# Optimization experiments

Hardware: AMD Instinct MI355X
Metric: run time of the kernel (lower is better)

The kernel has to match this reference:

```python
import jax, jax.numpy as jnp
import numpy as np

EPS = 1e-6
PRED_LEN = 336
K_DETACH = 6

def expmap0(v):
    # tangent v [..., E] at Lorentz origin (k=1) -> point [..., E+1]
    r = jnp.linalg.norm(v, axis=-1, keepdims=True)
    x0 = jnp.cosh(r)
    scale = jnp.where(r > EPS, jnp.sinh(r) / jnp.maximum(r, EPS), 1.0)
    return jnp.concatenate([x0, scale * v], axis=-1)

def logmap0(x):
    # Lorentz point [..., E+1] -> tangent [..., E] at origin (k=1)
    x0 = jnp.clip(x[..., :1], 1.0, None)
    xs = x[..., 1:]
    r = jnp.arccosh(x0)
    n = jnp.linalg.norm(xs, axis=-1, keepdims=True)
    return r * xs / jnp.maximum(n, EPS)

def setup_inputs():
    key = jax.random.key(0)
    ks = jax.random.split(key, 16)
    B, T, C = 128, 2048, 128
    E, H, L = 32, 64, 2048
    w = lambda k, s: jax.random.normal(k, s, jnp.float32) * 0.02
    z = lambda s: jnp.zeros(s, jnp.float32)
    return dict(
        x=jax.random.normal(ks[0], (B, T, C), jnp.float32),
        We_trend=w(ks[1], (L, E)), be_trend=z((E,)),
        We_weekly=w(ks[2], (L, E)), be_weekly=z((E,)),
        We_daily=w(ks[3], (L, E)), be_daily=z((E,)),
        We_resid=w(ks[4], (L, E)), be_resid=z((E,)),
        Wd_in=w(ks[5], (E, H)), bd_in=z((H,)),
        Wd_gate=w(ks[6], (E, H)), bd_gate=z((H,)),
        Wd_out=w(ks[7], (H, E)), bd_out=z((E,)),
        Wr=w(ks[8], (E, C)), br=z((C,)),
    )

def _forward(x, We_trend, be_trend, We_weekly, be_weekly, We_daily, be_daily,
             We_resid, be_resid, Wd_in, bd_in, Wd_gate, bd_gate, Wd_out, bd_out, Wr, br):
    B, T, C = x.shape
    k = min(7, T // 4)
    if k > 1:
        xp = jnp.pad(x, ((0, 0), (k // 2, k // 2), (0, 0)), mode='edge')  # replicate pad on time
        cs = jnp.cumsum(xp, axis=1)
        cs = jnp.concatenate([jnp.zeros((B, 1, C), x.dtype), cs], axis=1)
        trend = (cs[:, k:, :] - cs[:, :-k, :]) / k  # avg_pool1d(kernel=k, stride=1) -> [B,T,C]
    else:
        trend = x
    residual = x - trend
    # only channel 0 is consumed downstream
    t0 = trend[:, :, 0]       # [B, T]
    r0 = residual[:, :, 0]    # weekly == daily == resid == residual[:, :, 0]
    # ParallelLorentzBlock: per-component lookback projection, tanh, sum, lift to Lorentz
    v = (jnp.tanh(t0 @ We_trend + be_trend)
         + jnp.tanh(r0 @ We_weekly + be_weekly)
         + jnp.tanh(r0 @ We_daily + be_daily)
         + jnp.tanh(r0 @ We_resid + be_resid))  # [B, E]
    z0 = expmap0(v)  # combined_h on Lorentz manifold [B, E+1]
    masks = ((jnp.arange(PRED_LEN) + 1) % K_DETACH) == 0

    def step(z, m):
        tv = logmap0(z)  # [B, E]
        u = jax.nn.silu(tv @ Wd_in + bd_in) * jax.nn.sigmoid(tv @ Wd_gate + bd_gate)  # gated Mamba-style update
        vn = tv + u @ Wd_out + bd_out
        zn = expmap0(vn)
        x_pred = logmap0(zn) @ Wr + br  # reconstruction head -> [B, C]
        zc = jnp.where(m, jax.lax.stop_gradient(zn), zn)  # periodic detach every K steps
        return zc, x_pred

    _, preds = jax.lax.scan(step, z0, masks)  # [pred_len, B, C]
    return jnp.transpose(preds, (1, 0, 2))    # [B, pred_len, C]

def reference(x, We_trend, be_trend, We_weekly, be_weekly, We_daily, be_daily,
              We_resid, be_resid, Wd_in, bd_in, Wd_gate, bd_gate, Wd_out, bd_out, Wr, br):
    return _forward(x, We_trend, be_trend, We_weekly, be_weekly, We_daily, be_daily,
                    We_resid, be_resid, Wd_in, bd_in, Wd_gate, bd_gate, Wd_out, bd_out, Wr, br)
```

## Files before the change

### kernel.cpp

```cpp
#include <hip/hip_runtime.h>

typedef float v2f __attribute__((ext_vector_type(2)));

#define T_LEN 2048
#define BB    128
#define CC    128
#define EE    32
#define HH    64
#define PRED  336
#define CH    16
#define NCH   21

__device__ __forceinline__ v2f mk2(float a, float b) { v2f t; t.x = a; t.y = b; return t; }

__global__ __launch_bounds__(128, 1) void fused_kernel(
    const float* __restrict__ x,
    const float* __restrict__ WeT,  const float* __restrict__ beT,
    const float* __restrict__ WeW,  const float* __restrict__ beW,
    const float* __restrict__ WeD,  const float* __restrict__ beD,
    const float* __restrict__ WeR,  const float* __restrict__ beR,
    const float* __restrict__ Wdin, const float* __restrict__ bdin,
    const float* __restrict__ Wdg,  const float* __restrict__ bdg,
    const float* __restrict__ Wdo,  const float* __restrict__ bdo,
    const float* __restrict__ Wr,   const float* __restrict__ br,
    float* __restrict__ out)
{
    __shared__ __align__(16) float s_x   [T_LEN + 6];
    __shared__ __align__(16) float s_tr  [T_LEN];
    __shared__ __align__(16) float s_rs  [T_LEN];
    __shared__ __align__(16) float s_part[4][16][32];
    __shared__ __align__(16) float s_red [4][32];
    __shared__ __align__(16) float s_v   [EE];
    __shared__ __align__(16) float s_u   [2][CH][HH];

    const int tid  = threadIdx.x;
    const int wid  = tid >> 6;
    const int lane = tid & 63;
    const int b    = blockIdx.x;
    const float* xb = x + (size_t)b * T_LEN * CC;

    for (int i = tid; i < T_LEN + 6; i += 128) {
        int t = i - 3;
        t = t < 0 ? 0 : (t > T_LEN - 1 ? T_LEN - 1 : t);
        s_x[i] = xb[(size_t)t * CC];
    }
    __syncthreads();

    for (int t = tid; t < T_LEN; t += 128) {
        float s = 0.f;
        #pragma unroll
        for (int j = 0; j < 7; ++j) s += s_x[t + j];
        float tm = s * (1.0f / 7.0f);
        s_tr[t] = tm;
        s_rs[t] = s_x[t + 3] - tm;
    }
    __syncthreads();

    {
        const int eq = tid & 7, tg = tid >> 3;
        float4 aT = {0,0,0,0}, aW = aT, aD = aT, aR = aT;
        const float4* WT4 = (const float4*)WeT;
        const float4* WW4 = (const float4*)WeW;
        const float4* WD4 = (const float4*)WeD;
        const float4* WR4 = (const float4*)WeR;
        #pragma unroll 4
        for (int j = 0; j < 128; ++j) {
            int t  = tg * 128 + j;
            int wi = t * 8 + eq;
            float trv = s_tr[t], rsv = s_rs[t];
            float4 w;
            w = WT4[wi]; aT.x += trv*w.x; aT.y += trv*w.y; aT.z += trv*w.z; aT.w += trv*w.w;
            w = WW4[wi]; aW.x += rsv*w.x; aW.y += rsv*w.y; aW.z += rsv*w.z; aW.w += rsv*w.w;
            w = WD4[wi]; aD.x += rsv*w.x; aD.y += rsv*w.y; aD.z += rsv*w.z; aD.w += rsv*w.w;
            w = WR4[wi]; aR.x += rsv*w.x; aR.y += rsv*w.y; aR.z += rsv*w.z; aR.w += rsv*w.w;
        }
        ((float4*)&s_part[0][tg][0])[eq] = aT;
        ((float4*)&s_part[1][tg][0])[eq] = aW;
        ((float4*)&s_part[2][tg][0])[eq] = aD;
        ((float4*)&s_part[3][tg][0])[eq] = aR;
    }
    __syncthreads();

    {
        const int m = tid >> 5, e = tid & 31;
        float s = 0.f;
        #pragma unroll
        for (int g = 0; g < 16; ++g) s += s_part[m][g][e];
        s_red[m][e] = s;
    }
    __syncthreads();

    if (tid < EE) {
        s_v[tid] = tanhf(s_red[0][tid] + beT[tid])
                 + tanhf(s_red[1][tid] + beW[tid])
                 + tanhf(s_red[2][tid] + beD[tid])
                 + tanhf(s_red[3][tid] + beR[tid]);
    }
    __syncthreads();

    if (wid == 0) {
        v2f wig[EE];
        #pragma unroll
        for (int e = 0; e < EE; ++e)
            wig[e] = mk2(Wdin[e * HH + lane], Wdg[e * HH + lane]);

        v2f m_ag[HH];
        #pragma unroll 2
        for (int k = 0; k < HH; ++k) {
            v2f m = mk2(0.f, 0.f);
            #pragma unroll
            for (int e = 0; e < EE; ++e) m += Wdo[k * EE + e] * wig[e];
            m_ag[k] = m;
        }
        v2f c_ag = mk2(0.f, 0.f);
        v2f ag   = mk2(bdin[lane], bdg[lane]);
        #pragma unroll
        for (int e = 0; e < EE; ++e) {
            c_ag += bdo[e]  * wig[e];
            ag   += s_v[e]  * wig[e];
        }

        for (int c = 0; c < NCH + 1; ++c) {
            if (c < NCH) {
                float* ring = &s_u[c & 1][0][0];
                #pragma unroll 2
                for (int i = 0; i < CH; ++i) {
                    float a = ag.x, g = ag.y;
                    float u = a * __builtin_amdgcn_rcpf(
                        (1.f + __expf(-a)) * (1.f + __expf(-g)));
                    ring[i * HH + lane] = u;
                    v2f acc0 = c_ag, acc1 = mk2(0.f,0.f),
                        acc2 = acc1, acc3 = acc1;
                    const float4* u4 = (const float4*)(ring + i * HH);
                    #pragma unroll
                    for (int k = 0; k < HH / 4; ++k) {
                        float4 q = u4[k];
                        acc0 += q.x * m_ag[4 * k    ];
                        acc1 += q.y * m_ag[4 * k + 1];
                        acc2 += q.z * m_ag[4 * k + 2];
                        acc3 += q.w * m_ag[4 * k + 3];
                    }
                    ag += (acc0 + acc1) + (acc2 + acc3);
                }
            }
            __syncthreads();
        }
    } else {
        v2f wr2[EE];
        #pragma unroll
        for (int e = 0; e < EE; ++e)
            wr2[e] = *(const v2f*)(Wr + e * CC + 2 * lane);

        v2f m_r[HH];
        #pragma unroll 2
        for (int k = 0; k < HH; ++k) {
            v2f m = mk2(0.f, 0.f);
            #pragma unroll
            for (int e = 0; e < EE; ++e) m += Wdo[k * EE + e] * wr2[e];
            m_r[k] = m;
        }
        v2f c_r = mk2(0.f, 0.f);
        v2f P   = *(const v2f*)(br + 2 * lane);
        #pragma unroll
        for (int e = 0; e < EE; ++e) {
            c_r += bdo[e] * wr2[e];
            P   += s_v[e] * wr2[e];
        }

        float* outb = out + (size_t)b * PRED * CC + 2 * lane;

        for (int c = 0; c < NCH + 1; ++c) {
            if (c > 0) {
                const float* ring = &s_u[(c - 1) & 1][0][0];
                const int n0 = (c - 1) * CH;
                #pragma unroll 2
                for (int i = 0; i < CH; ++i) {
                    v2f acc0 = c_r, acc1 = mk2(0.f,0.f),
                        acc2 = acc1, acc3 = acc1;
                    const float4* u4 = (const float4*)(ring + i * HH);
                    #pragma unroll
                    for (int k = 0; k < HH / 4; ++k) {
                        float4 q = u4[k];
                        acc0 += q.x * m_r[4 * k    ];
                        acc1 += q.y * m_r[4 * k + 1];
                        acc2 += q.z * m_r[4 * k + 2];
                        acc3 += q.w * m_r[4 * k + 3];
                    }
                    P += (acc0 + acc1) + (acc2 + acc3);
                    *(v2f*)(outb + (size_t)(n0 + i) * CC) = P;
                }
            }
            __syncthreads();
        }
    }
}

extern "C" void kernel_launch(void* const* d_in, const int* in_sizes, int n_in,
                              void* d_out, int out_size, void* d_ws, size_t ws_size,
                              hipStream_t stream)
{
    const float* x    = (const float*)d_in[0];
    const float* WeT  = (const float*)d_in[1];
    const float* beT  = (const float*)d_in[2];
    const float* WeW  = (const float*)d_in[3];
    const float* beW  = (const float*)d_in[4];
    const float* WeD  = (const float*)d_in[5];
    const float* beD  = (const float*)d_in[6];
    const float* WeR  = (const float*)d_in[7];
    const float* beR  = (const float*)d_in[8];
    const float* Wdin = (const float*)d_in[9];
    const float* bdin = (const float*)d_in[10];
    const float* Wdg  = (const float*)d_in[11];
    const float* bdg  = (const float*)d_in[12];
    const float* Wdo  = (const float*)d_in[13];
    const float* bdo  = (const float*)d_in[14];
    const float* Wr   = (const float*)d_in[15];
    const float* br   = (const float*)d_in[16];

    fused_kernel<<<BB, 128, 0, stream>>>(x, WeT, beT, WeW, beW, WeD, beD,
                                         WeR, beR, Wdin, bdin, Wdg, bdg,
                                         Wdo, bdo, Wr, br, (float*)d_out);
}
```

Baseline: 407.7 us.

## Widen block to 256 threads, use readlane broadcast in recurrence, split output head

Doubles the block to 256 threads. This halves the per-thread length of the encoder projection loop and pads the trend and residual shared arrays to avoid bank conflicts. The recurrent warp now broadcasts u across lanes with readlane instead of reading it back from shared memory. The output head is split across two waves that each own 64 channels in scalar form, while the fourth wave only joins the barriers. The goal is to shorten the serial critical path and the per-wave work, at the cost of more registers per lane in the readlane loop and an idle wave.

```diff
diff --git a/kernel.cpp b/kernel.cpp
--- a/kernel.cpp
+++ b/kernel.cpp
@@ -11,9 +11,14 @@
 #define CH    16
 #define NCH   21
 
+#define PADT(t) ((t) + ((t) >> 7))
+
 __device__ __forceinline__ v2f mk2(float a, float b) { v2f t; t.x = a; t.y = b; return t; }
-
-__global__ __launch_bounds__(128, 1) void fused_kernel(
+__device__ __forceinline__ float rl(float v, int j) {
+    return __int_as_float(__builtin_amdgcn_readlane(__float_as_int(v), j));
+}
+
+__global__ __launch_bounds__(256, 1) void fused_kernel(
     const float* __restrict__ x,
     const float* __restrict__ WeT,  const float* __restrict__ beT,
     const float* __restrict__ WeW,  const float* __restrict__ beW,
@@ -26,9 +31,9 @@
     float* __restrict__ out)
 {
     __shared__ __align__(16) float s_x   [T_LEN + 6];
-    __shared__ __align__(16) float s_tr  [T_LEN];
-    __shared__ __align__(16) float s_rs  [T_LEN];
-    __shared__ __align__(16) float s_part[4][16][32];
+    __shared__ __align__(16) float s_tr  [T_LEN + 16];
+    __shared__ __align__(16) float s_rs  [T_LEN + 16];
+    __shared__ __align__(16) float s_part[4][32][32];
     __shared__ __align__(16) float s_red [4][32];
     __shared__ __align__(16) float s_v   [EE];
     __shared__ __align__(16) float s_u   [2][CH][HH];
@@ -39,20 +44,20 @@
     const int b    = blockIdx.x;
     const float* xb = x + (size_t)b * T_LEN * CC;
 
-    for (int i = tid; i < T_LEN + 6; i += 128) {
+    for (int i = tid; i < T_LEN + 6; i += 256) {
         int t = i - 3;
         t = t < 0 ? 0 : (t > T_LEN - 1 ? T_LEN - 1 : t);
         s_x[i] = xb[(size_t)t * CC];
     }
     __syncthreads();
 
-    for (int t = tid; t < T_LEN; t += 128) {
+    for (int t = tid; t < T_LEN; t += 256) {
         float s = 0.f;
         #pragma unroll
         for (int j = 0; j < 7; ++j) s += s_x[t + j];
         float tm = s * (1.0f / 7.0f);
-        s_tr[t] = tm;
-        s_rs[t] = s_x[t + 3] - tm;
+        s_tr[PADT(t)] = tm;
+        s_rs[PADT(t)] = s_x[t + 3] - tm;
     }
     __syncthreads();
 
@@ -64,10 +69,10 @@
         const float4* WD4 = (const float4*)WeD;
         const float4* WR4 = (const float4*)WeR;
         #pragma unroll 4
-        for (int j = 0; j < 128; ++j) {
-            int t  = tg * 128 + j;
+        for (int j = 0; j < 64; ++j) {
+            int t  = tg * 64 + j;
             int wi = t * 8 + eq;
-            float trv = s_tr[t], rsv = s_rs[t];
+            float trv = s_tr[PADT(t)], rsv = s_rs[PADT(t)];
             float4 w;
             w = WT4[wi]; aT.x += trv*w.x; aT.y += trv*w.y; aT.z += trv*w.z; aT.w += trv*w.w;
             w = WW4[wi]; aW.x += rsv*w.x; aW.y += rsv*w.y; aW.z += rsv*w.z; aW.w += rsv*w.w;
@@ -81,11 +86,11 @@
     }
     __syncthreads();
 
-    {
+    if (tid < 128) {
         const int m = tid >> 5, e = tid & 31;
         float s = 0.f;
         #pragma unroll
-        for (int g = 0; g < 16; ++g) s += s_part[m][g][e];
+        for (int g = 0; g < 32; ++g) s += s_part[m][g][e];
         s_red[m][e] = s;
     }
     __syncthreads();
@@ -116,82 +121,79 @@
         v2f ag   = mk2(bdin[lane], bdg[lane]);
         #pragma unroll
         for (int e = 0; e < EE; ++e) {
-            c_ag += bdo[e]  * wig[e];
-            ag   += s_v[e]  * wig[e];
-        }
-
-        for (int c = 0; c < NCH + 1; ++c) {
+            c_ag += bdo[e] * wig[e];
+            ag   += s_v[e] * wig[e];
+        }
+
+        for (int c = 0; c <= NCH; ++c) {
             if (c < NCH) {
                 float* ring = &s_u[c & 1][0][0];
-                #pragma unroll 2
                 for (int i = 0; i < CH; ++i) {
                     float a = ag.x, g = ag.y;
                     float u = a * __builtin_amdgcn_rcpf(
                         (1.f + __expf(-a)) * (1.f + __expf(-g)));
                     ring[i * HH + lane] = u;
-                    v2f acc0 = c_ag, acc1 = mk2(0.f,0.f),
+
+                    v2f acc0 = c_ag, acc1 = mk2(0.f, 0.f),
                         acc2 = acc1, acc3 = acc1;
-                    const float4* u4 = (const float4*)(ring + i * HH);
                     #pragma unroll
-                    for (int k = 0; k < HH / 4; ++k) {
-                        float4 q = u4[k];
-                        acc0 += q.x * m_ag[4 * k    ];
-                        acc1 += q.y * m_ag[4 * k + 1];
-                        acc2 += q.z * m_ag[4 * k + 2];
-                        acc3 += q.w * m_ag[4 * k + 3];
+                    for (int j = 0; j < HH; j += 4) {
+                        acc0 += rl(u, j    ) * m_ag[j    ];
+                        acc1 += rl(u, j + 1) * m_ag[j + 1];
+                        acc2 += rl(u, j + 2) * m_ag[j + 2];
+                        acc3 += rl(u, j + 3) * m_ag[j + 3];
                     }
                     ag += (acc0 + acc1) + (acc2 + acc3);
                 }
             }
             __syncthreads();
         }
-    } else {
-        v2f wr2[EE];
-        #pragma unroll
-        for (int e = 0; e < EE; ++e)
-            wr2[e] = *(const v2f*)(Wr + e * CC + 2 * lane);
-
-        v2f m_r[HH];
+    } else if (wid <= 2) {
+        const int c0 = (wid - 1) * 64 + lane;
+        float wr[EE];
+        #pragma unroll
+        for (int e = 0; e < EE; ++e) wr[e] = Wr[e * CC + c0];
+
+        float m_r[HH];
         #pragma unroll 2
         for (int k = 0; k < HH; ++k) {
-            v2f m = mk2(0.f, 0.f);
+            float m = 0.f;
             #pragma unroll
-            for (int e = 0; e < EE; ++e) m += Wdo[k * EE + e] * wr2[e];
+            for (int e = 0; e < EE; ++e) m += Wdo[k * EE + e] * wr[e];
             m_r[k] = m;
         }
-        v2f c_r = mk2(0.f, 0.f);
-        v2f P   = *(const v2f*)(br + 2 * lane);
+        float c_r = 0.f, P = br[c0];
         #pragma unroll
         for (int e = 0; e < EE; ++e) {
-            c_r += bdo[e] * wr2[e];
-            P   += s_v[e] * wr2[e];
-        }
-
-        float* outb = out + (size_t)b * PRED * CC + 2 * lane;
-
-        for (int c = 0; c < NCH + 1; ++c) {
+            c_r += bdo[e] * wr[e];
+            P   += s_v[e] * wr[e];
+        }
+
+        float* outb = out + (size_t)b * PRED * CC + c0;
+
+        for (int c = 0; c <= NCH; ++c) {
             if (c > 0) {
                 const float* ring = &s_u[(c - 1) & 1][0][0];
                 const int n0 = (c - 1) * CH;
-                #pragma unroll 2
                 for (int i = 0; i < CH; ++i) {
-                    v2f acc0 = c_r, acc1 = mk2(0.f,0.f),
-                        acc2 = acc1, acc3 = acc1;
+                    float a0 = c_r, a1 = 0.f, a2 = 0.f, a3 = 0.f;
                     const float4* u4 = (const float4*)(ring + i * HH);
                     #pragma unroll
                     for (int k = 0; k < HH / 4; ++k) {
                         float4 q = u4[k];
-                        acc0 += q.x * m_r[4 * k    ];
-                        acc1 += q.y * m_r[4 * k + 1];
-                        acc2 += q.z * m_r[4 * k + 2];
-                        acc3 += q.w * m_r[4 * k + 3];
+                        a0 += q.x * m_r[4 * k    ];
+                        a1 += q.y * m_r[4 * k + 1];
+                        a2 += q.z * m_r[4 * k + 2];
+                        a3 += q.w * m_r[4 * k + 3];
                     }
-                    P += (acc0 + acc1) + (acc2 + acc3);
-                    *(v2f*)(outb + (size_t)(n0 + i) * CC) = P;
+                    P += (a0 + a1) + (a2 + a3);
+                    outb[(size_t)(n0 + i) * CC] = P;
                 }
             }
             __syncthreads();
         }
+    } else {
+        for (int c = 0; c <= NCH; ++c) __syncthreads();
     }
 }
 
@@ -217,7 +219,7 @@
     const float* Wr   = (const float*)d_in[15];
     const float* br   = (const float*)d_in[16];
 
-    fused_kernel<<<BB, 128, 0, stream>>>(x, WeT, beT, WeW, beW, WeD, beD,
+    fused_kernel<<<BB, 256, 0, stream>>>(x, WeT, beT, WeW, beW, WeD, beD,
                                          WeR, beR, Wdin, bdin, Wdg, bdg,
                                          Wdo, bdo, Wr, br, (float*)d_out);
 }
```

New measurement: 434.7 us. 1.07x slower.
